# Performance work log

Hardware: AMD Instinct MI355X
Metric: run time of the kernel (lower is better)

The kernel has to match this reference:

```python
import jax, jax.numpy as jnp
import numpy as np

SEQ = 4096
EMB = 1024
OUT = 1024


def setup_inputs() -> dict:
    key = jax.random.key(0)
    k_x, k_q, k_k, k_v = jax.random.split(key, 4)
    scale = 1.0 / np.sqrt(EMB)
    inputs = jax.random.normal(k_x, (SEQ, EMB), dtype=jnp.float32)
    # torch Linear weight is (out_features, in_features); y = x @ W.T
    W_Q = jax.random.normal(k_q, (OUT, EMB), dtype=jnp.float32) * scale
    W_K = jax.random.normal(k_k, (OUT, EMB), dtype=jnp.float32) * scale
    W_V = jax.random.normal(k_v, (OUT, EMB), dtype=jnp.float32) * scale
    return {"inputs": inputs, "W_Q": W_Q, "W_K": W_K, "W_V": W_V}


def reference(inputs, W_Q, W_K, W_V):
    # projections: (S, E) @ (E, D) -> (S, D)
    q = inputs @ W_Q.T
    k = inputs @ W_K.T
    v = inputs @ W_V.T
    d_k = k.shape[-1]
    scores = (q @ k.T) / jnp.sqrt(jnp.asarray(d_k, dtype=q.dtype))  # (S, S)
    weights = jax.nn.softmax(scores, axis=-1)
    return weights @ v  # (S, D)
```

## Files before the change

### kernel.cpp

```cpp
#include <hip/hip_runtime.h>

typedef __bf16 bf16;
typedef __bf16 bf16x4 __attribute__((ext_vector_type(4)));
typedef __bf16 bf16x8 __attribute__((ext_vector_type(8)));
typedef float f32x4 __attribute__((ext_vector_type(4)));

#define SEQ 4096
#define EMB 1024

__device__ __forceinline__ void async_copy16(void* lds, const void* g) {
    __builtin_amdgcn_global_load_lds(
        (const __attribute__((address_space(1))) unsigned int*)g,
        (__attribute__((address_space(3))) unsigned int*)lds,
        16, 0, 0);
}

__global__ __launch_bounds__(256) void prep_all(const float* __restrict__ x,
                                                const float* __restrict__ wq,
                                                const float* __restrict__ wk,
                                                const float* __restrict__ wv,
                                                bf16* __restrict__ xb,
                                                bf16* __restrict__ wqk,
                                                bf16* __restrict__ wvb,
                                                float* __restrict__ rowsum)
{
    const int u = blockIdx.x * 256 + threadIdx.x;
    const float* src;
    bf16* dst;
    int off;
    if (u < 1048576)      { src = x;  dst = xb;               off = u; }
    else if (u < 1310720) { src = wq; dst = wqk;              off = u - 1048576; }
    else if (u < 1572864) { src = wk; dst = wqk + EMB * EMB;  off = u - 1310720; }
    else if (u < 1835008) { src = wv; dst = wvb;              off = u - 1572864; }
    else {
        *(float4*)(rowsum + (size_t)(u - 1835008) * 4) = float4{0.f, 0.f, 0.f, 0.f};
        return;
    }
    float4 f = *(const float4*)(src + (size_t)off * 4);
    bf16x4 v = { (bf16)f.x, (bf16)f.y, (bf16)f.z, (bf16)f.w };
    *(bf16x4*)(dst + (size_t)off * 4) = v;
}

template<bool RSUM>
__device__ __forceinline__ void gemm_core(const bf16* __restrict__ A,
                                          const bf16* __restrict__ B,
                                          int lda, int ldb, int K, long koff,
                                          int m0, int n0,
                                          bf16* __restrict__ As, bf16* __restrict__ Bs,
                                          f32x4 (&acc)[4][4], float (&rsum)[4],
                                          bool rs_active)
{
    const int tid  = threadIdx.x;
    const int lane = tid & 63;
    const int wave = tid >> 6;
    const int srow = tid >> 3;
    const int spc  = tid & 7;
    const int sl   = (spc - (srow & 7)) & 7;
    const int wm = (wave & 1) << 6;
    const int wn = (wave >> 1) << 6;
    const int fr = lane & 15;
    const int q  = lane >> 4;

    for (int i = 0; i < 4; i++)
        for (int j = 0; j < 4; j++)
            acc[i][j] = {0.f, 0.f, 0.f, 0.f};
    if (RSUM)
        for (int i = 0; i < 4; i++) rsum[i] = 0.f;

    const bf16* Ab = A + (size_t)(m0 + srow) * lda + koff + sl * 8;
    const bf16* Bb = B + (size_t)(n0 + srow) * ldb + koff + sl * 8;
    bf16* AsD = &As[srow * 64 + spc * 8];
    bf16* BsD = &Bs[srow * 64 + spc * 8];

    const int pc0 = ((q + fr) & 7) * 8;
    const int pc1 = pc0 ^ 32;

    for (int k0 = 0; k0 < K; k0 += 64) {
        __syncthreads();
        for (int t = 0; t < 4; t++) {
            async_copy16(AsD + t * 2048, Ab + k0 + (size_t)(32 * t) * lda);
            async_copy16(BsD + t * 2048, Bb + k0 + (size_t)(32 * t) * ldb);
        }
        __syncthreads();

        bf16x8 af[4], bg[4];
        for (int i = 0; i < 4; i++)
            af[i] = *(const bf16x8*)&As[(wm + i * 16 + fr) * 64 + pc0];
        for (int j = 0; j < 4; j++)
            bg[j] = *(const bf16x8*)&Bs[(wn + j * 16 + fr) * 64 + pc0];
        if (RSUM && rs_active)
            for (int i = 0; i < 4; i++)
                for (int e = 0; e < 8; e++) rsum[i] += (float)af[i][e];
        for (int i = 0; i < 4; i++)
            for (int j = 0; j < 4; j++)
                acc[i][j] = __builtin_amdgcn_mfma_f32_16x16x32_bf16(af[i], bg[j], acc[i][j], 0, 0, 0);

        for (int i = 0; i < 4; i++)
            af[i] = *(const bf16x8*)&As[(wm + i * 16 + fr) * 64 + pc1];
        for (int j = 0; j < 4; j++)
            bg[j] = *(const bf16x8*)&Bs[(wn + j * 16 + fr) * 64 + pc1];
        if (RSUM && rs_active)
            for (int i = 0; i < 4; i++)
                for (int e = 0; e < 8; e++) rsum[i] += (float)af[i][e];
        for (int i = 0; i < 4; i++)
            for (int j = 0; j < 4; j++)
                acc[i][j] = __builtin_amdgcn_mfma_f32_16x16x32_bf16(af[i], bg[j], acc[i][j], 0, 0, 0);
    }
}

__global__ __launch_bounds__(256) void gemm_proj(const bf16* __restrict__ xb,
                                                 const bf16* __restrict__ wqk,
                                                 const bf16* __restrict__ wvb,
                                                 bf16* __restrict__ QK,
                                                 bf16* __restrict__ VT)
{
    __shared__ __align__(16) bf16 As[128 * 64];
    __shared__ __align__(16) bf16 Bs[128 * 64];

    const bf16 *A, *B;
    bf16* C;
    int ldc, m0, n0;
    if (blockIdx.y < 16) {
        A = xb; B = wqk; C = QK; ldc = 2048;
        m0 = blockIdx.x * 128; n0 = blockIdx.y * 128;
    } else {
        A = wvb; B = xb; C = VT; ldc = 4096;
        m0 = (blockIdx.x & 7) * 128;
        n0 = ((blockIdx.x >> 3) + ((blockIdx.y - 16) << 2)) * 128;
    }

    f32x4 acc[4][4];
    float rs[4];
    gemm_core<false>(A, B, 1024, 1024, 1024, 0, m0, n0, As, Bs, acc, rs, false);

    const int lane = threadIdx.x & 63;
    const int wave = threadIdx.x >> 6;
    const int cm = m0 + ((wave & 1) << 6) + ((lane >> 4) << 2);
    const int cn = n0 + ((wave >> 1) << 6) + (lane & 15);
    for (int i = 0; i < 4; i++)
        for (int j = 0; j < 4; j++)
            for (int r = 0; r < 4; r++)
                C[(size_t)(cm + i * 16 + r) * ldc + (cn + j * 16)] = (bf16)acc[i][j][r];
}

__global__ __launch_bounds__(256) void gemm_exp(const bf16* __restrict__ QK,
                                                bf16* __restrict__ E)
{
    __shared__ __align__(16) bf16 As[128 * 64];
    __shared__ __align__(16) bf16 Bs[128 * 64];

    const int m0 = blockIdx.x * 128;
    const int n0 = blockIdx.y * 128;
    f32x4 acc[4][4];
    float rs[4];
    gemm_core<false>(QK, QK + 1024, 2048, 2048, 1024, 0, m0, n0, As, Bs, acc, rs, false);

    const int lane = threadIdx.x & 63;
    const int wave = threadIdx.x >> 6;
    const int cm = m0 + ((wave & 1) << 6) + ((lane >> 4) << 2);
    const int cn = n0 + ((wave >> 1) << 6) + (lane & 15);
    for (int i = 0; i < 4; i++)
        for (int j = 0; j < 4; j++)
            for (int r = 0; r < 4; r++)
                E[(size_t)(cm + i * 16 + r) * 4096 + (cn + j * 16)] =
                    (bf16)__expf(acc[i][j][r] * 0.03125f);
}

__global__ __launch_bounds__(256) void gemm_pv(const bf16* __restrict__ E,
                                               const bf16* __restrict__ VT,
                                               float* __restrict__ out,
                                               float* __restrict__ p1,
                                               float* __restrict__ rowsum)
{
    __shared__ __align__(16) bf16 As[128 * 64];
    __shared__ __align__(16) bf16 Bs[128 * 64];

    const int m0 = blockIdx.x * 128;
    const int n0 = blockIdx.y * 128;
    const long koff = (long)blockIdx.z * 1024;
    const bool rs_active = (blockIdx.y == 0) && (threadIdx.x < 128);

    f32x4 acc[4][4];
    float rs[4];
    gemm_core<true>(E, VT, 4096, 4096, 1024, koff, m0, n0, As, Bs, acc, rs, rs_active);

    const int lane = threadIdx.x & 63;
    const int wave = threadIdx.x >> 6;
    if (rs_active) {
        for (int i = 0; i < 4; i++) {
            rs[i] += __shfl_xor(rs[i], 16);
            rs[i] += __shfl_xor(rs[i], 32);
        }
        if (lane < 16) {
            const int wm = (wave & 1) << 6;
            for (int i = 0; i < 4; i++)
                unsafeAtomicAdd(&rowsum[m0 + wm + i * 16 + lane], rs[i]);
        }
    }

    float* C = (blockIdx.z == 0) ? out : p1 + (size_t)(blockIdx.z - 1) * SEQ * 1024;
    const int cm = m0 + ((wave & 1) << 6) + ((lane >> 4) << 2);
    const int cn = n0 + ((wave >> 1) << 6) + (lane & 15);
    for (int i = 0; i < 4; i++)
        for (int j = 0; j < 4; j++)
            for (int r = 0; r < 4; r++)
                C[(size_t)(cm + i * 16 + r) * 1024 + (cn + j * 16)] = acc[i][j][r];
}

__global__ __launch_bounds__(256) void reduce_norm(float* __restrict__ out,
                                                   const float* __restrict__ p1,
                                                   const float* __restrict__ p2,
                                                   const float* __restrict__ p3,
                                                   const float* __restrict__ rowsum)
{
    const int m = blockIdx.x;
    const float inv = 1.f / rowsum[m];
    const size_t off = (size_t)m * 1024 + threadIdx.x * 4;
    float4 a = *(const float4*)(out + off);
    float4 b = *(const float4*)(p1 + off);
    float4 c = *(const float4*)(p2 + off);
    float4 d = *(const float4*)(p3 + off);
    float4 o;
    o.x = (a.x + b.x + c.x + d.x) * inv;
    o.y = (a.y + b.y + c.y + d.y) * inv;
    o.z = (a.z + b.z + c.z + d.z) * inv;
    o.w = (a.w + b.w + c.w + d.w) * inv;
    *(float4*)(out + off) = o;
}

extern "C" void kernel_launch(void* const* d_in, const int* in_sizes, int n_in,
                              void* d_out, int out_size, void* d_ws, size_t ws_size,
                              hipStream_t stream)
{
    const float* x  = (const float*)d_in[0];
    const float* wq = (const float*)d_in[1];
    const float* wk = (const float*)d_in[2];
    const float* wv = (const float*)d_in[3];
    float* out = (float*)d_out;

    char* ws = (char*)d_ws;
    const size_t MB = 1024 * 1024;
    bf16*  E   = (bf16*)(ws);
    float* p1  = (float*)(ws + 32 * MB);
    float* p2  = (float*)(ws + 48 * MB);
    float* p3  = (float*)(ws + 64 * MB);
    bf16*  xb  = (bf16*)(ws + 32 * MB);
    bf16*  wqk = (bf16*)(ws + 40 * MB);
    bf16*  wvb = (bf16*)(ws + 44 * MB);
    bf16*  QK  = (bf16*)(ws + 64 * MB);
    bf16*  VT  = (bf16*)(ws + 80 * MB);
    float* rsm = (float*)(ws + 88 * MB);

    dim3 blk(256);

    prep_all<<<dim3(7172), blk, 0, stream>>>(x, wq, wk, wv, xb, wqk, wvb, rsm);
    gemm_proj<<<dim3(32, 24), blk, 0, stream>>>(xb, wqk, wvb, QK, VT);
    gemm_exp<<<dim3(32, 32), blk, 0, stream>>>(QK, E);
    gemm_pv<<<dim3(32, 8, 4), blk, 0, stream>>>(E, VT, out, p1, rsm);
    reduce_norm<<<dim3(4096), blk, 0, stream>>>(out, p1, p2, p3, rsm);
}
```

Measured before the change: 212.4 us.

## Switch GEMMs to 256x256 tiles with double-buffered async LDS loads

Replaces the 128x128 single-buffered GEMM core with a 256x256 tile computed by 8 waves (512 threads). Global-to-LDS async copies are double-buffered so the next K-slice loads while the current one feeds MFMA, with waitcnt and barrier placement and setprio around the MFMA bursts. The larger tile cuts global and LDS traffic per FLOP. The cost is fewer blocks, which underfills 256 CUs (gemm_proj 192 blocks, gemm_pv 256), plus higher register pressure and 128KB of LDS per block.

```diff
diff --git a/kernel.cpp b/kernel.cpp
--- a/kernel.cpp
+++ b/kernel.cpp
@@ -42,167 +42,219 @@
 }
 
 template<bool RSUM>
-__device__ __forceinline__ void gemm_core(const bf16* __restrict__ A,
-                                          const bf16* __restrict__ B,
-                                          int lda, int ldb, int K, long koff,
-                                          int m0, int n0,
-                                          bf16* __restrict__ As, bf16* __restrict__ Bs,
-                                          f32x4 (&acc)[4][4], float (&rsum)[4],
-                                          bool rs_active)
+__device__ __forceinline__ void tile_compute(const bf16* __restrict__ As,
+                                             const bf16* __restrict__ Bs,
+                                             int wr, int wc, int fr, int q,
+                                             f32x4 (&acc)[8][4], float (&rsum)[8],
+                                             bool rs_active)
+{
+    const int pc0 = ((q + fr) & 7) * 8;
+    const int pc1 = pc0 ^ 32;
+
+    bf16x8 bg[4][2];
+#pragma unroll
+    for (int nf = 0; nf < 4; nf++) {
+        const bf16* bp = Bs + (wc * 64 + nf * 16 + fr) * 64;
+        bg[nf][0] = *(const bf16x8*)(bp + pc0);
+        bg[nf][1] = *(const bf16x8*)(bp + pc1);
+    }
+#pragma unroll
+    for (int mg = 0; mg < 2; mg++) {
+        bf16x8 af[4][2];
+#pragma unroll
+        for (int mf = 0; mf < 4; mf++) {
+            const bf16* ap = As + (wr * 128 + mg * 64 + mf * 16 + fr) * 64;
+            af[mf][0] = *(const bf16x8*)(ap + pc0);
+            af[mf][1] = *(const bf16x8*)(ap + pc1);
+        }
+        if (RSUM && rs_active) {
+#pragma unroll
+            for (int mf = 0; mf < 4; mf++)
+#pragma unroll
+                for (int kh = 0; kh < 2; kh++)
+#pragma unroll
+                    for (int e = 0; e < 8; e++)
+                        rsum[mg * 4 + mf] += (float)af[mf][kh][e];
+        }
+        __builtin_amdgcn_s_setprio(1);
+#pragma unroll
+        for (int nf = 0; nf < 4; nf++)
+#pragma unroll
+            for (int mf = 0; mf < 4; mf++) {
+                f32x4 c = acc[mg * 4 + mf][nf];
+                c = __builtin_amdgcn_mfma_f32_16x16x32_bf16(af[mf][0], bg[nf][0], c, 0, 0, 0);
+                c = __builtin_amdgcn_mfma_f32_16x16x32_bf16(af[mf][1], bg[nf][1], c, 0, 0, 0);
+                acc[mg * 4 + mf][nf] = c;
+            }
+        __builtin_amdgcn_s_setprio(0);
+    }
+}
+
+template<bool RSUM>
+__device__ __forceinline__ void gemm_core256(const bf16* __restrict__ A,
+                                             const bf16* __restrict__ B,
+                                             int lda, int ldb, long koff,
+                                             int m0, int n0,
+                                             bf16* __restrict__ As,
+                                             bf16* __restrict__ Bs,
+                                             f32x4 (&acc)[8][4], float (&rsum)[8],
+                                             bool rs_active)
 {
     const int tid  = threadIdx.x;
     const int lane = tid & 63;
     const int wave = tid >> 6;
+    const int wr = wave >> 2;
+    const int wc = wave & 3;
     const int srow = tid >> 3;
     const int spc  = tid & 7;
     const int sl   = (spc - (srow & 7)) & 7;
-    const int wm = (wave & 1) << 6;
-    const int wn = (wave >> 1) << 6;
     const int fr = lane & 15;
     const int q  = lane >> 4;
 
-    for (int i = 0; i < 4; i++)
-        for (int j = 0; j < 4; j++)
-            acc[i][j] = {0.f, 0.f, 0.f, 0.f};
+#pragma unroll
+    for (int i = 0; i < 8; i++)
+#pragma unroll
+        for (int j = 0; j < 4; j++) acc[i][j] = {0.f, 0.f, 0.f, 0.f};
     if (RSUM)
-        for (int i = 0; i < 4; i++) rsum[i] = 0.f;
+#pragma unroll
+        for (int i = 0; i < 8; i++) rsum[i] = 0.f;
 
     const bf16* Ab = A + (size_t)(m0 + srow) * lda + koff + sl * 8;
     const bf16* Bb = B + (size_t)(n0 + srow) * ldb + koff + sl * 8;
-    bf16* AsD = &As[srow * 64 + spc * 8];
-    bf16* BsD = &Bs[srow * 64 + spc * 8];
-
-    const int pc0 = ((q + fr) & 7) * 8;
-    const int pc1 = pc0 ^ 32;
-
-    for (int k0 = 0; k0 < K; k0 += 64) {
-        __syncthreads();
-        for (int t = 0; t < 4; t++) {
-            async_copy16(AsD + t * 2048, Ab + k0 + (size_t)(32 * t) * lda);
-            async_copy16(BsD + t * 2048, Bb + k0 + (size_t)(32 * t) * ldb);
-        }
-        __syncthreads();
-
-        bf16x8 af[4], bg[4];
-        for (int i = 0; i < 4; i++)
-            af[i] = *(const bf16x8*)&As[(wm + i * 16 + fr) * 64 + pc0];
-        for (int j = 0; j < 4; j++)
-            bg[j] = *(const bf16x8*)&Bs[(wn + j * 16 + fr) * 64 + pc0];
-        if (RSUM && rs_active)
-            for (int i = 0; i < 4; i++)
-                for (int e = 0; e < 8; e++) rsum[i] += (float)af[i][e];
-        for (int i = 0; i < 4; i++)
-            for (int j = 0; j < 4; j++)
-                acc[i][j] = __builtin_amdgcn_mfma_f32_16x16x32_bf16(af[i], bg[j], acc[i][j], 0, 0, 0);
-
-        for (int i = 0; i < 4; i++)
-            af[i] = *(const bf16x8*)&As[(wm + i * 16 + fr) * 64 + pc1];
-        for (int j = 0; j < 4; j++)
-            bg[j] = *(const bf16x8*)&Bs[(wn + j * 16 + fr) * 64 + pc1];
-        if (RSUM && rs_active)
-            for (int i = 0; i < 4; i++)
-                for (int e = 0; e < 8; e++) rsum[i] += (float)af[i][e];
-        for (int i = 0; i < 4; i++)
-            for (int j = 0; j < 4; j++)
-                acc[i][j] = __builtin_amdgcn_mfma_f32_16x16x32_bf16(af[i], bg[j], acc[i][j], 0, 0, 0);
-    }
-}
-
-__global__ __launch_bounds__(256) void gemm_proj(const bf16* __restrict__ xb,
-                                                 const bf16* __restrict__ wqk,
-                                                 const bf16* __restrict__ wvb,
-                                                 bf16* __restrict__ QK,
-                                                 bf16* __restrict__ VT)
-{
-    __shared__ __align__(16) bf16 As[128 * 64];
-    __shared__ __align__(16) bf16 Bs[128 * 64];
+    bf16* AsD = As + srow * 64 + spc * 8;
+    bf16* BsD = Bs + srow * 64 + spc * 8;
+
+#pragma unroll
+    for (int u = 0; u < 4; u++) {
+        async_copy16(AsD + u * 4096, Ab + (size_t)(64 * u) * lda);
+        async_copy16(BsD + u * 4096, Bb + (size_t)(64 * u) * ldb);
+    }
+
+    for (int t = 0; t < 15; t++) {
+        const int p = t & 1;
+        const long kk = (long)(t + 1) * 64;
+#pragma unroll
+        for (int u = 0; u < 4; u++) {
+            async_copy16(AsD + (1 - p) * 16384 + u * 4096, Ab + kk + (size_t)(64 * u) * lda);
+            async_copy16(BsD + (1 - p) * 16384 + u * 4096, Bb + kk + (size_t)(64 * u) * ldb);
+        }
+        asm volatile("s_waitcnt vmcnt(8)" ::: "memory");
+        __builtin_amdgcn_s_barrier();
+        tile_compute<RSUM>(As + p * 16384, Bs + p * 16384, wr, wc, fr, q, acc, rsum, rs_active);
+        asm volatile("" ::: "memory");
+        __builtin_amdgcn_s_barrier();
+    }
+    asm volatile("s_waitcnt vmcnt(0)" ::: "memory");
+    __builtin_amdgcn_s_barrier();
+    tile_compute<RSUM>(As + 16384, Bs + 16384, wr, wc, fr, q, acc, rsum, rs_active);
+}
+
+__global__ __launch_bounds__(512, 2) void gemm_proj(const bf16* __restrict__ xb,
+                                                    const bf16* __restrict__ wqk,
+                                                    const bf16* __restrict__ wvb,
+                                                    bf16* __restrict__ QK,
+                                                    bf16* __restrict__ VT)
+{
+    __shared__ __align__(16) bf16 As[2][16384];
+    __shared__ __align__(16) bf16 Bs[2][16384];
 
     const bf16 *A, *B;
     bf16* C;
     int ldc, m0, n0;
-    if (blockIdx.y < 16) {
+    if (blockIdx.y < 8) {
         A = xb; B = wqk; C = QK; ldc = 2048;
-        m0 = blockIdx.x * 128; n0 = blockIdx.y * 128;
+        m0 = blockIdx.x * 256; n0 = blockIdx.y * 256;
     } else {
+        const int id = blockIdx.x + (blockIdx.y - 8) * 16;
         A = wvb; B = xb; C = VT; ldc = 4096;
-        m0 = (blockIdx.x & 7) * 128;
-        n0 = ((blockIdx.x >> 3) + ((blockIdx.y - 16) << 2)) * 128;
-    }
-
-    f32x4 acc[4][4];
-    float rs[4];
-    gemm_core<false>(A, B, 1024, 1024, 1024, 0, m0, n0, As, Bs, acc, rs, false);
+        m0 = (id & 3) * 256; n0 = (id >> 2) * 256;
+    }
+
+    f32x4 acc[8][4];
+    float rs[8];
+    gemm_core256<false>(A, B, 1024, 1024, 0, m0, n0, &As[0][0], &Bs[0][0], acc, rs, false);
 
     const int lane = threadIdx.x & 63;
     const int wave = threadIdx.x >> 6;
-    const int cm = m0 + ((wave & 1) << 6) + ((lane >> 4) << 2);
-    const int cn = n0 + ((wave >> 1) << 6) + (lane & 15);
-    for (int i = 0; i < 4; i++)
+    const int cm = m0 + (wave >> 2) * 128 + ((lane >> 4) << 2);
+    const int cn = n0 + (wave & 3) * 64 + (lane & 15);
+#pragma unroll
+    for (int i = 0; i < 8; i++)
+#pragma unroll
         for (int j = 0; j < 4; j++)
+#pragma unroll
             for (int r = 0; r < 4; r++)
                 C[(size_t)(cm + i * 16 + r) * ldc + (cn + j * 16)] = (bf16)acc[i][j][r];
 }
 
-__global__ __launch_bounds__(256) void gemm_exp(const bf16* __restrict__ QK,
-                                                bf16* __restrict__ E)
-{
-    __shared__ __align__(16) bf16 As[128 * 64];
-    __shared__ __align__(16) bf16 Bs[128 * 64];
-
-    const int m0 = blockIdx.x * 128;
-    const int n0 = blockIdx.y * 128;
-    f32x4 acc[4][4];
-    float rs[4];
-    gemm_core<false>(QK, QK + 1024, 2048, 2048, 1024, 0, m0, n0, As, Bs, acc, rs, false);
+__global__ __launch_bounds__(512, 2) void gemm_exp(const bf16* __restrict__ QK,
+                                                   bf16* __restrict__ E)
+{
+    __shared__ __align__(16) bf16 As[2][16384];
+    __shared__ __align__(16) bf16 Bs[2][16384];
+
+    const int m0 = blockIdx.x * 256;
+    const int n0 = blockIdx.y * 256;
+    f32x4 acc[8][4];
+    float rs[8];
+    gemm_core256<false>(QK, QK + 1024, 2048, 2048, 0, m0, n0, &As[0][0], &Bs[0][0], acc, rs, false);
 
     const int lane = threadIdx.x & 63;
     const int wave = threadIdx.x >> 6;
-    const int cm = m0 + ((wave & 1) << 6) + ((lane >> 4) << 2);
-    const int cn = n0 + ((wave >> 1) << 6) + (lane & 15);
-    for (int i = 0; i < 4; i++)
+    const int cm = m0 + (wave >> 2) * 128 + ((lane >> 4) << 2);
+    const int cn = n0 + (wave & 3) * 64 + (lane & 15);
+#pragma unroll
+    for (int i = 0; i < 8; i++)
+#pragma unroll
         for (int j = 0; j < 4; j++)
+#pragma unroll
             for (int r = 0; r < 4; r++)
                 E[(size_t)(cm + i * 16 + r) * 4096 + (cn + j * 16)] =
                     (bf16)__expf(acc[i][j][r] * 0.03125f);
 }
 
-__global__ __launch_bounds__(256) void gemm_pv(const bf16* __restrict__ E,
-                                               const bf16* __restrict__ VT,
-                                               float* __restrict__ out,
-                                               float* __restrict__ p1,
-                                               float* __restrict__ rowsum)
-{
-    __shared__ __align__(16) bf16 As[128 * 64];
-    __shared__ __align__(16) bf16 Bs[128 * 64];
-
-    const int m0 = blockIdx.x * 128;
-    const int n0 = blockIdx.y * 128;
+__global__ __launch_bounds__(512, 2) void gemm_pv(const bf16* __restrict__ E,
+                                                  const bf16* __restrict__ VT,
+                                                  float* __restrict__ out,
+                                                  float* __restrict__ p1,
+                                                  float* __restrict__ rowsum)
+{
+    __shared__ __align__(16) bf16 As[2][16384];
+    __shared__ __align__(16) bf16 Bs[2][16384];
+
+    const int m0 = blockIdx.x * 256;
+    const int n0 = blockIdx.y * 256;
     const long koff = (long)blockIdx.z * 1024;
-    const bool rs_active = (blockIdx.y == 0) && (threadIdx.x < 128);
-
-    f32x4 acc[4][4];
-    float rs[4];
-    gemm_core<true>(E, VT, 4096, 4096, 1024, koff, m0, n0, As, Bs, acc, rs, rs_active);
+    const bool rs_active = (blockIdx.y == 0) && (((threadIdx.x >> 6) & 3) == 0);
+
+    f32x4 acc[8][4];
+    float rs[8];
+    gemm_core256<true>(E, VT, 4096, 4096, koff, m0, n0, &As[0][0], &Bs[0][0], acc, rs, rs_active);
 
     const int lane = threadIdx.x & 63;
     const int wave = threadIdx.x >> 6;
     if (rs_active) {
-        for (int i = 0; i < 4; i++) {
+#pragma unroll
+        for (int i = 0; i < 8; i++) {
             rs[i] += __shfl_xor(rs[i], 16);
             rs[i] += __shfl_xor(rs[i], 32);
         }
         if (lane < 16) {
-            const int wm = (wave & 1) << 6;
-            for (int i = 0; i < 4; i++)
-                unsafeAtomicAdd(&rowsum[m0 + wm + i * 16 + lane], rs[i]);
+            const int rbase = m0 + (wave >> 2) * 128;
+#pragma unroll
+            for (int i = 0; i < 8; i++)
+                unsafeAtomicAdd(&rowsum[rbase + i * 16 + lane], rs[i]);
         }
     }
 
     float* C = (blockIdx.z == 0) ? out : p1 + (size_t)(blockIdx.z - 1) * SEQ * 1024;
-    const int cm = m0 + ((wave & 1) << 6) + ((lane >> 4) << 2);
-    const int cn = n0 + ((wave >> 1) << 6) + (lane & 15);
-    for (int i = 0; i < 4; i++)
+    const int cm = m0 + (wave >> 2) * 128 + ((lane >> 4) << 2);
+    const int cn = n0 + (wave & 3) * 64 + (lane & 15);
+#pragma unroll
+    for (int i = 0; i < 8; i++)
+#pragma unroll
         for (int j = 0; j < 4; j++)
+#pragma unroll
             for (int r = 0; r < 4; r++)
                 C[(size_t)(cm + i * 16 + r) * 1024 + (cn + j * 16)] = acc[i][j][r];
 }
@@ -251,11 +303,9 @@
     bf16*  VT  = (bf16*)(ws + 80 * MB);
     float* rsm = (float*)(ws + 88 * MB);
 
-    dim3 blk(256);
-
-    prep_all<<<dim3(7172), blk, 0, stream>>>(x, wq, wk, wv, xb, wqk, wvb, rsm);
-    gemm_proj<<<dim3(32, 24), blk, 0, stream>>>(xb, wqk, wvb, QK, VT);
-    gemm_exp<<<dim3(32, 32), blk, 0, stream>>>(QK, E);
-    gemm_pv<<<dim3(32, 8, 4), blk, 0, stream>>>(E, VT, out, p1, rsm);
-    reduce_norm<<<dim3(4096), blk, 0, stream>>>(out, p1, p2, p3, rsm);
-}
+    prep_all<<<dim3(7172), dim3(256), 0, stream>>>(x, wq, wk, wv, xb, wqk, wvb, rsm);
+    gemm_proj<<<dim3(16, 12), dim3(512), 0, stream>>>(xb, wqk, wvb, QK, VT);
+    gemm_exp<<<dim3(16, 16), dim3(512), 0, stream>>>(QK, E);
+    gemm_pv<<<dim3(16, 4, 4), dim3(512), 0, stream>>>(E, VT, out, p1, rsm);
+    reduce_norm<<<dim3(4096), dim3(256), 0, stream>>>(out, p1, p2, p3, rsm);
+}
```

Measured after the change: 211.4 us. Within noise of the previous version (-0.5%).
